# Kernel optimization log

Hardware: AMD Instinct MI355X
Metric: run time of the kernel (lower is better)

Reference implementation:

```python
import jax, jax.numpy as jnp
import numpy as np

N_HEAD = 32
N_KV_HEAD = 8
HEAD_DIM = 64
ROPE_BASE = 10000.0


def _rope_tables(T, dim):
    inv_freq = 1.0 / (ROPE_BASE ** (jnp.arange(0, dim, 2, dtype=jnp.float32) / dim))
    t = jnp.arange(T, dtype=jnp.float32)
    freqs = jnp.outer(t, inv_freq)            # [T, dim/2]
    emb = jnp.concatenate([freqs, freqs], -1)  # [T, dim]
    return jnp.cos(emb), jnp.sin(emb)


def _rotate_half(x):
    x1, x2 = jnp.split(x, 2, axis=-1)
    return jnp.concatenate([-x2, x1], axis=-1)


def setup_inputs() -> dict:
    key = jax.random.key(0)
    ks = jax.random.split(key, 5)
    B, T, C = 2, 2048, 2048
    kv_dim = N_KV_HEAD * HEAD_DIM
    s = 0.02
    return {
        "x":  jax.random.normal(ks[0], (B, T, C), jnp.float32),
        "Wq": jax.random.normal(ks[1], (C, C), jnp.float32) * s,
        "Wk": jax.random.normal(ks[2], (C, kv_dim), jnp.float32) * s,
        "Wv": jax.random.normal(ks[3], (C, kv_dim), jnp.float32) * s,
        "Wo": jax.random.normal(ks[4], (C, C), jnp.float32) * s,
    }


def reference(x, Wq, Wk, Wv, Wo):
    B, T, C = x.shape
    n_rep = N_HEAD // N_KV_HEAD  # 4 query heads per KV head

    q = (x @ Wq).reshape(B, T, N_HEAD, HEAD_DIM).transpose(0, 2, 1, 3)      # [B,H,T,d]
    k = (x @ Wk).reshape(B, T, N_KV_HEAD, HEAD_DIM).transpose(0, 2, 1, 3)   # [B,Hk,T,d]
    v = (x @ Wv).reshape(B, T, N_KV_HEAD, HEAD_DIM).transpose(0, 2, 1, 3)   # [B,Hk,T,d]

    cos, sin = _rope_tables(T, HEAD_DIM)  # [T,d], broadcast over batch/heads
    q = q * cos + _rotate_half(q) * sin
    k = k * cos + _rotate_half(k) * sin

    # group Q heads by their shared KV head (equivalent to repeat_interleave on K/V)
    qg = q.reshape(B, N_KV_HEAD, n_rep, T, HEAD_DIM)
    scale = 1.0 / np.sqrt(HEAD_DIM).astype(np.float32)
    att = jnp.einsum('bgrtd,bgsd->bgrts', qg, k) * scale  # [B,Hk,rep,T,T]

    causal = jnp.tril(jnp.ones((T, T), dtype=bool))
    att = jnp.where(causal, att, -jnp.inf)
    att = jax.nn.softmax(att, axis=-1)

    y = jnp.einsum('bgrts,bgsd->bgrtd', att, v)            # [B,Hk,rep,T,d]
    y = y.reshape(B, N_HEAD, T, HEAD_DIM).transpose(0, 2, 1, 3).reshape(B, T, C)
    return y @ Wo
```

## Files before the change

kernel.cpp:

```cpp
#include <hip/hip_runtime.h>
#include <hip/hip_bf16.h>
#include <math.h>

#define B_SZ    2
#define T_SEQ   2048
#define C_DIM   2048
#define N_HEAD  32
#define N_KVH   8
#define HDIM    64
#define KV_DIM  (N_KVH * HDIM)
#define M_ROWS  (B_SZ * T_SEQ)
#define RLN     0.28782313662425575f

typedef __bf16 bf16x8 __attribute__((ext_vector_type(8)));
typedef float f32x4 __attribute__((ext_vector_type(4)));
typedef unsigned short u16x4 __attribute__((ext_vector_type(4)));
typedef unsigned short u16x8 __attribute__((ext_vector_type(8)));

__device__ inline unsigned short f2bf(float f) {
    __bf16 h = (__bf16)f;
    return __builtin_bit_cast(unsigned short, h);
}


__global__ __launch_bounds__(256) void convert_a(const float* __restrict__ A,
                                                 unsigned short* __restrict__ Ab,
                                                 int K) {
    const int t = blockIdx.x >> 1, half = blockIdx.x & 1;
    const int ktiles = K >> 5;
    const int mt = t / ktiles, kt = t % ktiles;
    const int m  = threadIdx.x >> 1;
    const int ks = half * 2 + (threadIdx.x & 1);

    const float* src = A + (size_t)(mt * 128 + m) * K + kt * 32 + ks * 8;
    const float4 a = *(const float4*)src;
    const float4 b = *(const float4*)(src + 4);
    u16x8 o;
    o[0] = f2bf(a.x); o[1] = f2bf(a.y); o[2] = f2bf(a.z); o[3] = f2bf(a.w);
    o[4] = f2bf(b.x); o[5] = f2bf(b.y); o[6] = f2bf(b.z); o[7] = f2bf(b.w);
    const int g = ks * 128 + m;
    *(u16x8*)(Ab + ((size_t)t * 512 + g) * 8) = o;
}

__global__ __launch_bounds__(256) void convert_w(const float* __restrict__ W,
                                                 unsigned short* __restrict__ Wb,
                                                 int K, int N) {
    const int t = blockIdx.x >> 1, half = blockIdx.x & 1;
    const int ktiles = K >> 5;
    const int nt = t / ktiles, kt = t % ktiles;
    const int g  = half * 256 + threadIdx.x;
    const int nn = g & 127, ks = g >> 7;

    const float* src = W + (size_t)(kt * 32 + ks * 8) * N + nt * 128 + nn;
    u16x8 o;
    #pragma unroll
    for (int j = 0; j < 8; ++j) o[j] = f2bf(src[(size_t)j * N]);
    *(u16x8*)(Wb + ((size_t)t * 512 + g) * 8) = o;
}

#define GEMM_BODY()                                                             \
    __shared__ __align__(16) unsigned short As[4096];                           \
    __shared__ __align__(16) unsigned short Bs[4096];                           \
    const int tid  = threadIdx.x;                                               \
    const int wave = tid >> 6, lane = tid & 63;                                 \
    const int quad = lane >> 4, l15 = lane & 15;                                \
    const int wr = wave >> 1, wc = wave & 1;                                    \
    const int ktiles = K >> 5;                                                  \
    const unsigned short* Atile = Ab + (size_t)blockIdx.y * ktiles * 4096;      \
    const unsigned short* Btile = Bb + (size_t)blockIdx.x * ktiles * 4096;      \
    f32x4 acc[4][4];                                                            \
    _Pragma("unroll")                                                           \
    for (int i = 0; i < 4; ++i)                                                 \
        _Pragma("unroll")                                                       \
        for (int j = 0; j < 4; ++j) acc[i][j] = (f32x4){0.f, 0.f, 0.f, 0.f};   \
    for (int kt = 0; kt < ktiles; ++kt) {                                       \
        {                                                                       \
            const unsigned short* gsrc = (wave < 2 ? Atile : Btile) + (size_t)kt * 4096; \
            unsigned short* ldst = (wave < 2 ? As : Bs);                        \
            const int s0 = (wave & 1) * 4;                                      \
            _Pragma("unroll")                                                   \
            for (int u = 0; u < 4; ++u) {                                       \
                const int seg = s0 + u;                                         \
                __builtin_amdgcn_global_load_lds(                               \
                    (const __attribute__((address_space(1))) unsigned int*)(gsrc + seg * 512 + lane * 8), \
                    (__attribute__((address_space(3))) unsigned int*)(ldst + seg * 512), \
                    16, 0, 0);                                                  \
            }                                                                   \
        }                                                                       \
        __syncthreads();                                                        \
        bf16x8 af[4], bfr[4];                                                   \
        _Pragma("unroll")                                                       \
        for (int i = 0; i < 4; ++i)                                             \
            af[i] = *(const bf16x8*)&As[quad * 1024 + (wr * 64 + i * 16 + l15) * 8]; \
        _Pragma("unroll")                                                       \
        for (int j = 0; j < 4; ++j)                                             \
            bfr[j] = *(const bf16x8*)&Bs[quad * 1024 + (wc * 64 + j * 16 + l15) * 8]; \
        _Pragma("unroll")                                                       \
        for (int i = 0; i < 4; ++i)                                             \
            _Pragma("unroll")                                                   \
            for (int j = 0; j < 4; ++j)                                         \
                acc[i][j] = __builtin_amdgcn_mfma_f32_16x16x32_bf16(af[i], bfr[j], acc[i][j], 0, 0, 0); \
        __syncthreads();                                                        \
    }

__global__ __launch_bounds__(256) void gemm_bf16(const unsigned short* __restrict__ Ab,
                                                 const unsigned short* __restrict__ Bb,
                                                 float* __restrict__ C,
                                                 int M, int N, int K) {
    GEMM_BODY()
    const int m0 = blockIdx.y * 128 + wr * 64 + quad * 4;
    const int n0 = blockIdx.x * 128 + wc * 64 + l15;
    #pragma unroll
    for (int i = 0; i < 4; ++i)
        #pragma unroll
        for (int r = 0; r < 4; ++r) {
            const int row = m0 + i * 16 + r;
            #pragma unroll
            for (int j = 0; j < 4; ++j)
                C[(size_t)row * N + n0 + j * 16] = acc[i][j][r];
        }
}

__global__ __launch_bounds__(256) void gemm_bf16_qkv(const unsigned short* __restrict__ Ab,
                                                     const unsigned short* __restrict__ Bb,
                                                     unsigned short* __restrict__ Qb,
                                                     unsigned short* __restrict__ Kbuf,
                                                     unsigned short* __restrict__ Vt,
                                                     int K) {
    GEMM_BODY()
    const int nblk = blockIdx.x * 128;
    const int m0   = blockIdx.y * 128 + wr * 64 + quad * 4;
    const int colw = nblk + wc * 64;

    if (nblk < 2048) {
        const int h = colw >> 6;
        const float invf0 = __expf(-(float)l15 * RLN);
        const float invf1 = __expf(-(float)(l15 + 16) * RLN);
        #pragma unroll
        for (int i = 0; i < 4; ++i)
            #pragma unroll
            for (int r = 0; r < 4; ++r) {
                const int row = m0 + i * 16 + r;
                const float t = (float)(row & (T_SEQ - 1));
                float s0, c0, s1, c1;
                sincosf(t * invf0, &s0, &c0);
                sincosf(t * invf1, &s1, &c1);
                const float x0 = acc[i][0][r], x1 = acc[i][1][r];
                const float x2 = acc[i][2][r], x3 = acc[i][3][r];
                unsigned short* dst = Qb + (size_t)row * C_DIM + h * HDIM + l15;
                dst[0]  = f2bf((x0 * c0 - x2 * s0) * 0.125f);
                dst[16] = f2bf((x1 * c1 - x3 * s1) * 0.125f);
                dst[32] = f2bf((x2 * c0 + x0 * s0) * 0.125f);
                dst[48] = f2bf((x3 * c1 + x1 * s1) * 0.125f);
            }
    } else if (nblk < 2560) {
        const int kvh = (colw - 2048) >> 6;
        const float invf0 = __expf(-(float)l15 * RLN);
        const float invf1 = __expf(-(float)(l15 + 16) * RLN);
        const int c8l = l15 >> 3, dil = l15 & 7;
        #pragma unroll
        for (int i = 0; i < 4; ++i)
            #pragma unroll
            for (int r = 0; r < 4; ++r) {
                const int row = m0 + i * 16 + r;
                const int tt = row & (T_SEQ - 1);
                const int bb = row >> 11;
                const float t = (float)tt;
                float s0, c0, s1, c1;
                sincosf(t * invf0, &s0, &c0);
                sincosf(t * invf1, &s1, &c1);
                const float x0 = acc[i][0][r], x1 = acc[i][1][r];
                const float x2 = acc[i][2][r], x3 = acc[i][3][r];
                unsigned short* dst = Kbuf + (size_t)((bb * N_KVH + kvh) * 64 + (tt >> 5)) * 2048;
                const int kk = tt & 31;
                dst[((c8l + 0) * 32 + kk) * 8 + dil] = f2bf(x0 * c0 - x2 * s0);
                dst[((c8l + 2) * 32 + kk) * 8 + dil] = f2bf(x1 * c1 - x3 * s1);
                dst[((c8l + 4) * 32 + kk) * 8 + dil] = f2bf(x2 * c0 + x0 * s0);
                dst[((c8l + 6) * 32 + kk) * 8 + dil] = f2bf(x3 * c1 + x1 * s1);
            }
    } else {
        const int kvh = (colw - 2560) >> 6;
        const int bb = m0 >> 11;
        #pragma unroll
        for (int i = 0; i < 4; ++i) {
            const int t0 = (m0 + i * 16) & (T_SEQ - 1);
            const int tile = t0 >> 5, o = (t0 >> 3) & 3, i8 = t0 & 7;
            unsigned short* dst = Vt + (size_t)((bb * N_KVH + kvh) * 64 + tile) * 2048;
            #pragma unroll
            for (int j = 0; j < 4; ++j) {
                const int d = j * 16 + l15;
                u16x4 pk;
                pk[0] = f2bf(acc[i][j][0]); pk[1] = f2bf(acc[i][j][1]);
                pk[2] = f2bf(acc[i][j][2]); pk[3] = f2bf(acc[i][j][3]);
                *(u16x4*)(dst + (o * 64 + d) * 8 + i8) = pk;
            }
        }
    }
}

__global__ __launch_bounds__(256, 2) void attn_mfma(const unsigned short* __restrict__ Qb,
                                                    const unsigned short* __restrict__ Kbuf,
                                                    const unsigned short* __restrict__ Vt,
                                                    unsigned short* __restrict__ Yb) {
    __shared__ __align__(16) unsigned short Ks[2][4096];
    __shared__ __align__(16) unsigned short Vs[2][4096];
    __shared__ __align__(16) unsigned short Ps[4][1152];

    const int bid = blockIdx.x;
    const int qb  = 7 - (bid >> 6);
    const int hs  = bid & 63;
    const int h   = hs & 31;
    const int b   = hs >> 5;
    const int kvh = h >> 2;
    const int q0  = qb << 8;

    const int tid  = threadIdx.x;
    const int wave = tid >> 6, lane = tid & 63;
    const int quad = lane >> 4, l15 = lane & 15;
    const int qw   = q0 + wave * 64;
    const int jd   = qb * 4 + wave;
    const int jtmax = qb * 4 + 3;

    bf16x8 qf[4][2];
    #pragma unroll
    for (int mt = 0; mt < 4; ++mt) {
        const size_t qoff = (size_t)(b * T_SEQ + qw + mt * 16 + l15) * C_DIM + h * HDIM + quad * 8;
        qf[mt][0] = *(const bf16x8*)(Qb + qoff);
        qf[mt][1] = *(const bf16x8*)(Qb + qoff + 32);
    }

    const unsigned short* kbase = Kbuf + (size_t)((b * N_KVH + kvh) * 64) * 2048;
    const unsigned short* vbase = Vt + (size_t)((b * N_KVH + kvh) * 64) * 2048;

    f32x4 acc[4][4];
    #pragma unroll
    for (int mt = 0; mt < 4; ++mt)
        #pragma unroll
        for (int c = 0; c < 4; ++c) acc[mt][c] = (f32x4){0.f, 0.f, 0.f, 0.f};
    float psum[4][4];
    #pragma unroll
    for (int mt = 0; mt < 4; ++mt)
        #pragma unroll
        for (int r = 0; r < 4; ++r) psum[mt][r] = 0.f;

    #define STAGE(JT, BUF)                                                         \
        {                                                                          \
            const unsigned short* gsrc = (wave < 2 ? kbase : vbase) + (size_t)(JT) * 4096; \
            unsigned short* ldst = (wave < 2 ? Ks[BUF] : Vs[BUF]);                 \
            const int s0 = (wave & 1) * 4;                                         \
            _Pragma("unroll")                                                      \
            for (int u = 0; u < 4; ++u) {                                          \
                const int seg = s0 + u;                                            \
                __builtin_amdgcn_global_load_lds(                                  \
                    (const __attribute__((address_space(1))) unsigned int*)(gsrc + seg * 512 + lane * 8), \
                    (__attribute__((address_space(3))) unsigned int*)(ldst + seg * 512), \
                    16, 0, 0);                                                     \
            }                                                                      \
        }

    STAGE(0, 0)

    for (int jt = 0; jt <= jtmax; ++jt) {
        __syncthreads();
        if (jt < jtmax) STAGE(jt + 1, (jt + 1) & 1)

        if (jt <= jd) {
            const unsigned short* Ksb = Ks[jt & 1];
            const unsigned short* Vsb = Vs[jt & 1];
            const int j0 = jt << 6;

            bf16x8 kf[4][2], vf[2][4];
            #pragma unroll
            for (int st = 0; st < 4; ++st)
                #pragma unroll
                for (int c = 0; c < 2; ++c)
                    kf[st][c] = *(const bf16x8*)
                        &Ksb[(st >> 1) * 2048 + ((c * 4 + quad) * 32 + (st & 1) * 16 + l15) * 8];
            #pragma unroll
            for (int kc = 0; kc < 2; ++kc)
                #pragma unroll
                for (int c = 0; c < 4; ++c)
                    vf[kc][c] = *(const bf16x8*)
                        &Vsb[kc * 2048 + (quad * 64 + c * 16 + l15) * 8];

            const bool diag = (jt == jd);
            #pragma unroll
            for (int mt = 0; mt < 4; ++mt) {
                f32x4 sacc[4];
                #pragma unroll
                for (int st = 0; st < 4; ++st) {
                    f32x4 s = (f32x4){0.f, 0.f, 0.f, 0.f};
                    s = __builtin_amdgcn_mfma_f32_16x16x32_bf16(qf[mt][0], kf[st][0], s, 0, 0, 0);
                    s = __builtin_amdgcn_mfma_f32_16x16x32_bf16(qf[mt][1], kf[st][1], s, 0, 0, 0);
                    sacc[st] = s;
                }

                float p[4][4];
                if (!diag) {
                    #pragma unroll
                    for (int st = 0; st < 4; ++st)
                        #pragma unroll
                        for (int r = 0; r < 4; ++r)
                            p[st][r] = __expf(sacc[st][r]);
                } else {
                    #pragma unroll
                    for (int st = 0; st < 4; ++st)
                        #pragma unroll
                        for (int r = 0; r < 4; ++r) {
                            const int key = j0 + st * 16 + l15;
                            const int q   = qw + mt * 16 + quad * 4 + r;
                            p[st][r] = __expf(key > q ? -1e30f : sacc[st][r]);
                        }
                }
                #pragma unroll
                for (int r = 0; r < 4; ++r) {
                    #pragma unroll
                    for (int st = 0; st < 4; ++st)
                        Ps[wave][(quad * 4 + r) * 72 + st * 16 + l15] = f2bf(p[st][r]);
                    psum[mt][r] += (p[0][r] + p[1][r]) + (p[2][r] + p[3][r]);
                }

                #pragma unroll
                for (int kc = 0; kc < 2; ++kc) {
                    const bf16x8 pa = *(const bf16x8*)&Ps[wave][l15 * 72 + kc * 32 + quad * 8];
                    #pragma unroll
                    for (int c = 0; c < 4; ++c)
                        acc[mt][c] = __builtin_amdgcn_mfma_f32_16x16x32_bf16(pa, vf[kc][c], acc[mt][c], 0, 0, 0);
                }
            }
        }
    }
    #undef STAGE

    #pragma unroll
    for (int mt = 0; mt < 4; ++mt)
        #pragma unroll
        for (int r = 0; r < 4; ++r) {
            float s = psum[mt][r];
            #pragma unroll
            for (int off = 1; off < 16; off <<= 1) s += __shfl_xor(s, off, 16);
            const float inv = 1.0f / s;
            const int grow = b * T_SEQ + qw + mt * 16 + quad * 4 + r;
            const int mtt = grow >> 7, m = grow & 127;
            #pragma unroll
            for (int c = 0; c < 4; ++c) {
                const int col = h * HDIM + c * 16 + l15;
                const int kt = col >> 5, ks = (col >> 3) & 3, e = col & 7;
                Yb[(size_t)(mtt * 64 + kt) * 4096 + (ks * 128 + m) * 8 + e]
                    = f2bf(acc[mt][c][r] * inv);
            }
        }
}

extern "C" void kernel_launch(void* const* d_in, const int* in_sizes, int n_in,
                              void* d_out, int out_size, void* d_ws, size_t ws_size,
                              hipStream_t stream) {
    const float* x  = (const float*)d_in[0];
    const float* Wq = (const float*)d_in[1];
    const float* Wk = (const float*)d_in[2];
    const float* Wv = (const float*)d_in[3];
    const float* Wo = (const float*)d_in[4];

    char* base = (char*)d_ws;
    unsigned short* xb    = (unsigned short*)(base + 0);
    unsigned short* Wqkvb = (unsigned short*)(base + (16ull << 20));
    unsigned short* Wob   = (unsigned short*)(base + (28ull << 20));
    unsigned short* Qb    = (unsigned short*)(base + (36ull << 20));
    unsigned short* Kb    = (unsigned short*)(base + (52ull << 20));
    unsigned short* Vt    = (unsigned short*)(base + (56ull << 20));
    unsigned short* Yb    = xb;

    const dim3 blk(256);

    convert_a<<<(M_ROWS * C_DIM) / 2048, blk, 0, stream>>>(x, xb, C_DIM);
    convert_w<<<(C_DIM * C_DIM) / 2048, blk, 0, stream>>>(Wq, Wqkvb, C_DIM, C_DIM);
    convert_w<<<(C_DIM * KV_DIM) / 2048, blk, 0, stream>>>(Wk, Wqkvb + (size_t)1024 * 4096, C_DIM, KV_DIM);
    convert_w<<<(C_DIM * KV_DIM) / 2048, blk, 0, stream>>>(Wv, Wqkvb + (size_t)1280 * 4096, C_DIM, KV_DIM);
    convert_w<<<(C_DIM * C_DIM) / 2048, blk, 0, stream>>>(Wo, Wob, C_DIM, C_DIM);

    gemm_bf16_qkv<<<dim3(3072 / 128, M_ROWS / 128), blk, 0, stream>>>(xb, Wqkvb, Qb, Kb, Vt, C_DIM);

    attn_mfma<<<B_SZ * N_HEAD * (T_SEQ / 256), blk, 0, stream>>>(Qb, Kb, Vt, Yb);

    gemm_bf16<<<dim3(C_DIM / 128, M_ROWS / 128), blk, 0, stream>>>(Yb, Wob, (float*)d_out, M_ROWS, C_DIM, C_DIM);
}
```

Measured before the change: 322.3 us.

## Regroup attention blocks by KV head and read K/V fragments directly from global

Each block now handles one 64-row query chunk for all four query heads sharing a KV head, one head per wave, so K/V tiles are reused across the GQA group. LDS staging and the per-tile __syncthreads are gone; each wave loads K/V fragments straight from global (L1/L2), and the K/V layouts are repacked into 64-key tiles to suit those loads. Key ordering within a tile is permuted (l15*4+st) so P can be written to LDS as packed 4-element stores. The cost is more global/L2 traffic per wave and no explicit prefetch of the next tile, which may leave load latency exposed.

```diff
diff --git a/kernel.cpp b/kernel.cpp
--- a/kernel.cpp
+++ b/kernel.cpp
@@ -171,12 +171,12 @@
                 sincosf(t * invf1, &s1, &c1);
                 const float x0 = acc[i][0][r], x1 = acc[i][1][r];
                 const float x2 = acc[i][2][r], x3 = acc[i][3][r];
-                unsigned short* dst = Kbuf + (size_t)((bb * N_KVH + kvh) * 64 + (tt >> 5)) * 2048;
-                const int kk = tt & 31;
-                dst[((c8l + 0) * 32 + kk) * 8 + dil] = f2bf(x0 * c0 - x2 * s0);
-                dst[((c8l + 2) * 32 + kk) * 8 + dil] = f2bf(x1 * c1 - x3 * s1);
-                dst[((c8l + 4) * 32 + kk) * 8 + dil] = f2bf(x2 * c0 + x0 * s0);
-                dst[((c8l + 6) * 32 + kk) * 8 + dil] = f2bf(x3 * c1 + x1 * s1);
+                unsigned short* dst = Kbuf + (size_t)((bb * N_KVH + kvh) * 32 + (tt >> 6)) * 4096;
+                const int kk = tt & 63;
+                dst[((c8l + 0) * 64 + kk) * 8 + dil] = f2bf(x0 * c0 - x2 * s0);
+                dst[((c8l + 2) * 64 + kk) * 8 + dil] = f2bf(x1 * c1 - x3 * s1);
+                dst[((c8l + 4) * 64 + kk) * 8 + dil] = f2bf(x2 * c0 + x0 * s0);
+                dst[((c8l + 6) * 64 + kk) * 8 + dil] = f2bf(x3 * c1 + x1 * s1);
             }
     } else {
         const int kvh = (colw - 2560) >> 6;
@@ -184,8 +184,8 @@
         #pragma unroll
         for (int i = 0; i < 4; ++i) {
             const int t0 = (m0 + i * 16) & (T_SEQ - 1);
-            const int tile = t0 >> 5, o = (t0 >> 3) & 3, i8 = t0 & 7;
-            unsigned short* dst = Vt + (size_t)((bb * N_KVH + kvh) * 64 + tile) * 2048;
+            const int o = (t0 >> 3) & 7, i8 = t0 & 7;
+            unsigned short* dst = Vt + (size_t)((bb * N_KVH + kvh) * 32 + (t0 >> 6)) * 4096;
             #pragma unroll
             for (int j = 0; j < 4; ++j) {
                 const int d = j * 16 + l15;
@@ -202,24 +202,21 @@
                                                     const unsigned short* __restrict__ Kbuf,
                                                     const unsigned short* __restrict__ Vt,
                                                     unsigned short* __restrict__ Yb) {
-    __shared__ __align__(16) unsigned short Ks[2][4096];
-    __shared__ __align__(16) unsigned short Vs[2][4096];
     __shared__ __align__(16) unsigned short Ps[4][1152];
 
     const int bid = blockIdx.x;
-    const int qb  = 7 - (bid >> 6);
-    const int hs  = bid & 63;
-    const int h   = hs & 31;
-    const int b   = hs >> 5;
-    const int kvh = h >> 2;
-    const int q0  = qb << 8;
+    const int x   = bid & 7;
+    const int g   = bid >> 3;
+    const int combo = x * 2 + (g & 1);
+    const int qc  = 31 - (g >> 1);
+    const int b   = combo >> 3;
+    const int kvh = combo & 7;
 
     const int tid  = threadIdx.x;
     const int wave = tid >> 6, lane = tid & 63;
     const int quad = lane >> 4, l15 = lane & 15;
-    const int qw   = q0 + wave * 64;
-    const int jd   = qb * 4 + wave;
-    const int jtmax = qb * 4 + 3;
+    const int h    = kvh * 4 + wave;
+    const int qw   = qc * 64;
 
     bf16x8 qf[4][2];
     #pragma unroll
@@ -229,8 +226,8 @@
         qf[mt][1] = *(const bf16x8*)(Qb + qoff + 32);
     }
 
-    const unsigned short* kbase = Kbuf + (size_t)((b * N_KVH + kvh) * 64) * 2048;
-    const unsigned short* vbase = Vt + (size_t)((b * N_KVH + kvh) * 64) * 2048;
+    const unsigned short* kbase = Kbuf + (size_t)((b * N_KVH + kvh) * 32) * 4096;
+    const unsigned short* vbase = Vt + (size_t)((b * N_KVH + kvh) * 32) * 4096;
 
     f32x4 acc[4][4];
     #pragma unroll
@@ -243,94 +240,71 @@
         #pragma unroll
         for (int r = 0; r < 4; ++r) psum[mt][r] = 0.f;
 
-    #define STAGE(JT, BUF)                                                         \
-        {                                                                          \
-            const unsigned short* gsrc = (wave < 2 ? kbase : vbase) + (size_t)(JT) * 4096; \
-            unsigned short* ldst = (wave < 2 ? Ks[BUF] : Vs[BUF]);                 \
-            const int s0 = (wave & 1) * 4;                                         \
-            _Pragma("unroll")                                                      \
-            for (int u = 0; u < 4; ++u) {                                          \
-                const int seg = s0 + u;                                            \
-                __builtin_amdgcn_global_load_lds(                                  \
-                    (const __attribute__((address_space(1))) unsigned int*)(gsrc + seg * 512 + lane * 8), \
-                    (__attribute__((address_space(3))) unsigned int*)(ldst + seg * 512), \
-                    16, 0, 0);                                                     \
-            }                                                                      \
-        }
-
-    STAGE(0, 0)
-
-    for (int jt = 0; jt <= jtmax; ++jt) {
-        __syncthreads();
-        if (jt < jtmax) STAGE(jt + 1, (jt + 1) & 1)
-
-        if (jt <= jd) {
-            const unsigned short* Ksb = Ks[jt & 1];
-            const unsigned short* Vsb = Vs[jt & 1];
-            const int j0 = jt << 6;
-
-            bf16x8 kf[4][2], vf[2][4];
-            #pragma unroll
-            for (int st = 0; st < 4; ++st)
+    for (int jt = 0; jt <= qc; ++jt) {
+        const unsigned short* kt = kbase + (size_t)jt * 4096;
+        const unsigned short* vt = vbase + (size_t)jt * 4096;
+
+        bf16x8 kf[4][2], vf[2][4];
+        #pragma unroll
+        for (int st = 0; st < 4; ++st)
+            #pragma unroll
+            for (int c = 0; c < 2; ++c)
+                kf[st][c] = *(const bf16x8*)&kt[((c * 4 + quad) * 64 + l15 * 4 + st) * 8];
+        #pragma unroll
+        for (int kc = 0; kc < 2; ++kc)
+            #pragma unroll
+            for (int c = 0; c < 4; ++c)
+                vf[kc][c] = *(const bf16x8*)&vt[((kc * 4 + quad) * 64 + c * 16 + l15) * 8];
+
+        const bool diag = (jt == qc);
+        const int j0 = jt << 6;
+
+        #pragma unroll
+        for (int mt = 0; mt < 4; ++mt) {
+            f32x4 sacc[4];
+            #pragma unroll
+            for (int st = 0; st < 4; ++st) {
+                f32x4 s = (f32x4){0.f, 0.f, 0.f, 0.f};
+                s = __builtin_amdgcn_mfma_f32_16x16x32_bf16(qf[mt][0], kf[st][0], s, 0, 0, 0);
+                s = __builtin_amdgcn_mfma_f32_16x16x32_bf16(qf[mt][1], kf[st][1], s, 0, 0, 0);
+                sacc[st] = s;
+            }
+
+            float p[4][4];
+            if (!diag) {
                 #pragma unroll
-                for (int c = 0; c < 2; ++c)
-                    kf[st][c] = *(const bf16x8*)
-                        &Ksb[(st >> 1) * 2048 + ((c * 4 + quad) * 32 + (st & 1) * 16 + l15) * 8];
-            #pragma unroll
-            for (int kc = 0; kc < 2; ++kc)
+                for (int st = 0; st < 4; ++st)
+                    #pragma unroll
+                    for (int r = 0; r < 4; ++r)
+                        p[st][r] = __expf(sacc[st][r]);
+            } else {
+                #pragma unroll
+                for (int st = 0; st < 4; ++st)
+                    #pragma unroll
+                    for (int r = 0; r < 4; ++r) {
+                        const int key = j0 + l15 * 4 + st;
+                        const int q   = qw + mt * 16 + quad * 4 + r;
+                        p[st][r] = __expf(key > q ? -1e30f : sacc[st][r]);
+                    }
+            }
+            #pragma unroll
+            for (int r = 0; r < 4; ++r) {
+                u16x4 pk;
+                pk[0] = f2bf(p[0][r]); pk[1] = f2bf(p[1][r]);
+                pk[2] = f2bf(p[2][r]); pk[3] = f2bf(p[3][r]);
+                *(u16x4*)&Ps[wave][(quad * 4 + r) * 72 + l15 * 4] = pk;
+                psum[mt][r] += (p[0][r] + p[1][r]) + (p[2][r] + p[3][r]);
+            }
+
+            #pragma unroll
+            for (int kc = 0; kc < 2; ++kc) {
+                const bf16x8 pa = *(const bf16x8*)&Ps[wave][l15 * 72 + kc * 32 + quad * 8];
                 #pragma unroll
                 for (int c = 0; c < 4; ++c)
-                    vf[kc][c] = *(const bf16x8*)
-                        &Vsb[kc * 2048 + (quad * 64 + c * 16 + l15) * 8];
-
-            const bool diag = (jt == jd);
-            #pragma unroll
-            for (int mt = 0; mt < 4; ++mt) {
-                f32x4 sacc[4];
-                #pragma unroll
-                for (int st = 0; st < 4; ++st) {
-                    f32x4 s = (f32x4){0.f, 0.f, 0.f, 0.f};
-                    s = __builtin_amdgcn_mfma_f32_16x16x32_bf16(qf[mt][0], kf[st][0], s, 0, 0, 0);
-                    s = __builtin_amdgcn_mfma_f32_16x16x32_bf16(qf[mt][1], kf[st][1], s, 0, 0, 0);
-                    sacc[st] = s;
-                }
-
-                float p[4][4];
-                if (!diag) {
-                    #pragma unroll
-                    for (int st = 0; st < 4; ++st)
-                        #pragma unroll
-                        for (int r = 0; r < 4; ++r)
-                            p[st][r] = __expf(sacc[st][r]);
-                } else {
-                    #pragma unroll
-                    for (int st = 0; st < 4; ++st)
-                        #pragma unroll
-                        for (int r = 0; r < 4; ++r) {
-                            const int key = j0 + st * 16 + l15;
-                            const int q   = qw + mt * 16 + quad * 4 + r;
-                            p[st][r] = __expf(key > q ? -1e30f : sacc[st][r]);
-                        }
-                }
-                #pragma unroll
-                for (int r = 0; r < 4; ++r) {
-                    #pragma unroll
-                    for (int st = 0; st < 4; ++st)
-                        Ps[wave][(quad * 4 + r) * 72 + st * 16 + l15] = f2bf(p[st][r]);
-                    psum[mt][r] += (p[0][r] + p[1][r]) + (p[2][r] + p[3][r]);
-                }
-
-                #pragma unroll
-                for (int kc = 0; kc < 2; ++kc) {
-                    const bf16x8 pa = *(const bf16x8*)&Ps[wave][l15 * 72 + kc * 32 + quad * 8];
-                    #pragma unroll
-                    for (int c = 0; c < 4; ++c)
-                        acc[mt][c] = __builtin_amdgcn_mfma_f32_16x16x32_bf16(pa, vf[kc][c], acc[mt][c], 0, 0, 0);
-                }
+                    acc[mt][c] = __builtin_amdgcn_mfma_f32_16x16x32_bf16(pa, vf[kc][c], acc[mt][c], 0, 0, 0);
             }
         }
     }
-    #undef STAGE
 
     #pragma unroll
     for (int mt = 0; mt < 4; ++mt)
@@ -345,8 +319,8 @@
             #pragma unroll
             for (int c = 0; c < 4; ++c) {
                 const int col = h * HDIM + c * 16 + l15;
-                const int kt = col >> 5, ks = (col >> 3) & 3, e = col & 7;
-                Yb[(size_t)(mtt * 64 + kt) * 4096 + (ks * 128 + m) * 8 + e]
+                const int kt2 = col >> 5, ks = (col >> 3) & 3, e = col & 7;
+                Yb[(size_t)(mtt * 64 + kt2) * 4096 + (ks * 128 + m) * 8 + e]
                     = f2bf(acc[mt][c][r] * inv);
             }
         }
@@ -380,7 +354,7 @@
 
     gemm_bf16_qkv<<<dim3(3072 / 128, M_ROWS / 128), blk, 0, stream>>>(xb, Wqkvb, Qb, Kb, Vt, C_DIM);
 
-    attn_mfma<<<B_SZ * N_HEAD * (T_SEQ / 256), blk, 0, stream>>>(Qb, Kb, Vt, Yb);
+    attn_mfma<<<B_SZ * N_KVH * (T_SEQ / 64), blk, 0, stream>>>(Qb, Kb, Vt, Yb);
 
     gemm_bf16<<<dim3(C_DIM / 128, M_ROWS / 128), blk, 0, stream>>>(Yb, Wob, (float*)d_out, M_ROWS, C_DIM, C_DIM);
 }
```

New measurement: 309.9 us. 3.9% less time.
